# Kernel tuning notes

Hardware: AMD Instinct MI355X
Metric: run time of the kernel (lower is better)

Reference implementation:

```python
import jax, jax.numpy as jnp
import numpy as np


def setup_inputs() -> dict:
    key = jax.random.key(0)
    k1, k2, k3, k4, k5 = jax.random.split(key, 5)
    B, C, H, W = 8, 256, 64, 64
    Cp = C // 8  # query/key channels
    x = jax.random.normal(k1, (B, C, H, W), dtype=jnp.float32)
    # 1x1 conv weights (bias=False in the module), spectral norm treated as a fixed weight scale
    Wq = jax.random.normal(k2, (Cp, C), dtype=jnp.float32) * 0.05
    Wk = jax.random.normal(k3, (Cp, C), dtype=jnp.float32) * 0.05
    Wv = jax.random.normal(k4, (C, C), dtype=jnp.float32) * 0.05
    gamma = jax.random.normal(k5, (1,), dtype=jnp.float32)
    return {"x": x, "Wq": Wq, "Wk": Wk, "Wv": Wv, "gamma": gamma}


def reference(x, Wq, Wk, Wv, gamma):
    B, C, H, W = x.shape
    xf = x.reshape(B, C, H * W)  # (B, C, N)
    # ConvLayer = 1x1 conv (no bias) followed by ReLU
    f = jax.nn.relu(jnp.einsum('oc,bcn->bon', Wq, xf))  # (B, C', N)
    g = jax.nn.relu(jnp.einsum('oc,bcn->bon', Wk, xf))  # (B, C', N)
    h = jax.nn.relu(jnp.einsum('oc,bcn->bon', Wv, xf))  # (B, C, N)
    # beta = softmax(f^T g, dim=1): normalize over the FIRST N axis (faithful to source)
    scores = jnp.einsum('bcn,bcm->bnm', f, g)  # (B, N, N)
    beta = jax.nn.softmax(scores, axis=1)
    o = gamma * jnp.einsum('bcn,bnm->bcm', h, beta) + xf  # (B, C, N)
    return o.reshape(B, C, H, W)
```

## Files before the change

### kernel.cpp

```cpp
#include <hip/hip_runtime.h>


typedef __attribute__((ext_vector_type(8))) short bf16x8;
typedef __attribute__((ext_vector_type(4))) float f32x4;
typedef __attribute__((ext_vector_type(4))) unsigned short us4;

#define LOG2E 1.44269504088896f

static __device__ __forceinline__ unsigned short f2bf(float x) {
    union { float f; unsigned u; } v; v.f = x;
    unsigned r = v.u + 0x7FFFu + ((v.u >> 16) & 1u);
    return (unsigned short)(r >> 16);
}
static __device__ __forceinline__ float bf2f(unsigned short u) {
    union { unsigned u; float f; } v; v.u = ((unsigned)u) << 16;
    return v.f;
}

__global__ __launch_bounds__(256) void wconv_kernel(
    const float* __restrict__ Wq, const float* __restrict__ Wk,
    const float* __restrict__ Wv, unsigned short* __restrict__ wq,
    unsigned short* __restrict__ wk, unsigned short* __restrict__ wv)
{
    const int i = blockIdx.x * 256 + threadIdx.x;
    if (i < 8192)            wq[i] = f2bf(Wq[i] * LOG2E);
    else if (i < 16384)      wk[i - 8192] = f2bf(Wk[i - 8192]);
    else                     wv[i - 16384] = f2bf(Wv[i - 16384]);
}

#define XPITCH 264
#define HPITCH 72
__global__ __launch_bounds__(256, 2) void producer_kernel(
    const float* __restrict__ x, const unsigned short* __restrict__ wq,
    const unsigned short* __restrict__ wk, const unsigned short* __restrict__ wv,
    unsigned short* __restrict__ f_t, unsigned short* __restrict__ g_t,
    unsigned short* __restrict__ h_bf, float* __restrict__ normg,
    unsigned* __restrict__ maxnf_u)
{
    __shared__ unsigned short xh_s[256 * HPITCH];
    __shared__ unsigned short fg_s[4 * 2 * 512];

    const int tid  = threadIdx.x;
    const int w    = tid >> 6;
    const int lane = tid & 63;
    const int q    = lane >> 4;
    const int r    = lane & 15;
    const int b    = blockIdx.y;
    const int nt   = blockIdx.x;
    const int n0   = nt << 6;
    const size_t bN = (size_t)b << 12;
    const f32x4 zero = {0.f, 0.f, 0.f, 0.f};

#pragma unroll
    for (int jj = 0; jj < 4; jj++) {
        const int task = jj * 256 + tid;
        const int n4 = task & 15;
        const int c4 = task >> 4;
        float va[4][4];
#pragma unroll
        for (int i = 0; i < 4; i++) {
            const float4 v = ((const float4*)(x + ((size_t)b << 20)
                              + (size_t)(c4 * 4 + i) * 4096 + n0))[n4];
            va[i][0] = v.x; va[i][1] = v.y; va[i][2] = v.z; va[i][3] = v.w;
        }
#pragma unroll
        for (int i = 0; i < 4; i++) {
            us4 t;
            t.x = f2bf(va[0][i]); t.y = f2bf(va[1][i]);
            t.z = f2bf(va[2][i]); t.w = f2bf(va[3][i]);
            *(us4*)(xh_s + (n4 * 4 + i) * XPITCH + c4 * 4) = t;
        }
    }
    __syncthreads();

    f32x4 acch[4][4];
    f32x4 accf[2], accg[2];
#pragma unroll
    for (int cs = 0; cs < 4; cs++)
#pragma unroll
        for (int ns = 0; ns < 4; ns++) acch[cs][ns] = zero;
    accf[0] = accf[1] = accg[0] = accg[1] = zero;

    for (int ks = 0; ks < 8; ks++) {
        const int kof = ks * 32 + q * 8;
        bf16x8 av[4], aq[2], ak[2];
#pragma unroll
        for (int cs = 0; cs < 4; cs++)
            av[cs] = *(const bf16x8*)(wv + (size_t)(w * 64 + cs * 16 + r) * 256 + kof);
#pragma unroll
        for (int ms = 0; ms < 2; ms++) {
            aq[ms] = *(const bf16x8*)(wq + (size_t)(ms * 16 + r) * 256 + kof);
            ak[ms] = *(const bf16x8*)(wk + (size_t)(ms * 16 + r) * 256 + kof);
        }
#pragma unroll
        for (int ns = 0; ns < 4; ns++) {
            const bf16x8 bx = *(const bf16x8*)(xh_s + (ns * 16 + r) * XPITCH + kof);
#pragma unroll
            for (int cs = 0; cs < 4; cs++)
                acch[cs][ns] = __builtin_amdgcn_mfma_f32_16x16x32_bf16(av[cs], bx, acch[cs][ns], 0, 0, 0);
            if (ns == w) {
#pragma unroll
                for (int ms = 0; ms < 2; ms++) {
                    accf[ms] = __builtin_amdgcn_mfma_f32_16x16x32_bf16(aq[ms], bx, accf[ms], 0, 0, 0);
                    accg[ms] = __builtin_amdgcn_mfma_f32_16x16x32_bf16(ak[ms], bx, accg[ms], 0, 0, 0);
                }
            }
        }
    }

    unsigned short* lf = fg_s + w * 1024;
    unsigned short* lg = lf + 512;
#pragma unroll
    for (int ms = 0; ms < 2; ms++)
#pragma unroll
        for (int reg = 0; reg < 4; reg++) {
            lf[r * 32 + ms * 16 + q * 4 + reg] = f2bf(fmaxf(accf[ms][reg], 0.f));
            lg[r * 32 + ms * 16 + q * 4 + reg] = f2bf(fmaxf(accg[ms][reg], 0.f));
        }
    const bf16x8 ffrag = *(const bf16x8*)(lf + r * 32 + q * 8);
    const bf16x8 gfrag = *(const bf16x8*)(lg + r * 32 + q * 8);
    *(bf16x8*)(f_t + ((bN + n0 + w * 16 + r) << 5) + q * 8) = ffrag;
    *(bf16x8*)(g_t + ((bN + n0 + w * 16 + r) << 5) + q * 8) = gfrag;

    float nf2 = 0.f, ng2 = 0.f;
#pragma unroll
    for (int i = 0; i < 8; i++) {
        const float fv = bf2f(((unsigned short*)&ffrag)[i]);
        const float gv = bf2f(((unsigned short*)&gfrag)[i]);
        nf2 += fv * fv; ng2 += gv * gv;
    }
    nf2 += __shfl_xor(nf2, 16); nf2 += __shfl_xor(nf2, 32);
    ng2 += __shfl_xor(ng2, 16); ng2 += __shfl_xor(ng2, 32);
    if (q == 0) normg[bN + n0 + w * 16 + r] = sqrtf(ng2);
    float nf = sqrtf(nf2);
#pragma unroll
    for (int off = 1; off < 16; off <<= 1) nf = fmaxf(nf, __shfl_xor(nf, off));
    if (lane == 0) atomicMax(maxnf_u + b, __float_as_uint(nf));

    __syncthreads();
#pragma unroll
    for (int cs = 0; cs < 4; cs++)
#pragma unroll
        for (int ns = 0; ns < 4; ns++)
#pragma unroll
            for (int reg = 0; reg < 4; reg++)
                xh_s[(w * 64 + cs * 16 + q * 4 + reg) * HPITCH + ns * 16 + r] =
                    f2bf(fmaxf(acch[cs][ns][reg], 0.f));
    __syncthreads();
    const size_t hdst = ((size_t)(b * 64 + nt)) << 14;
#pragma unroll
    for (int p = 0; p < 8; p++) {
        const int c = p * 32 + (tid >> 3);
        const int k = tid & 7;
        *(bf16x8*)(h_bf + hdst + c * 64 + k * 8) =
            *(const bf16x8*)(xh_s + c * HPITCH + k * 8);
    }
}

__global__ __launch_bounds__(256, 2) void attn_kernel(
    const unsigned short* __restrict__ f_t, const unsigned short* __restrict__ g_t,
    const unsigned short* __restrict__ h_bf, const float* __restrict__ x,
    const float* __restrict__ gamma, const float* __restrict__ normg,
    const unsigned* __restrict__ maxnf_u, float* __restrict__ out)
{
    __shared__ unsigned short p_s[3][64 * 64];
    __shared__ float red_l[4][64];
    __shared__ float sLi[64];

    const int tid  = threadIdx.x;
    const int w    = tid >> 6;
    const int lane = tid & 63;
    const int q    = lane >> 4;
    const int r    = lane & 15;
    const int b    = blockIdx.y;
    const int m0   = blockIdx.x << 6;

    const size_t bN = (size_t)b << 12;
    const int c0 = w << 6;
    const f32x4 zero = {0.f, 0.f, 0.f, 0.f};

    bf16x8 bg[4];
    float nMh[4];
    const float mnf = __uint_as_float(maxnf_u[b]);
#pragma unroll
    for (int ms = 0; ms < 4; ms++) {
        bg[ms] = *(const bf16x8*)(g_t + ((bN + m0 + ms * 16 + r) << 5) + (q << 3));
        nMh[ms] = -(mnf * normg[bN + m0 + ms * 16 + r] * 1.0002f);
    }

    f32x4 acc[4][4];
#pragma unroll
    for (int cs = 0; cs < 4; cs++)
#pragma unroll
        for (int ms = 0; ms < 4; ms++) acc[cs][ms] = zero;
    float lt[4] = {0.f, 0.f, 0.f, 0.f};

    const int wkey = r & 7;
    const int wchunkoff = (((((w << 1) + (q >> 1)) ^ wkey) << 3)) + ((q & 1) << 2);
    const int rkoff0 = ((q ^ wkey) << 3);
    const int rkoff1 = (((4 + q) ^ wkey) << 3);

    auto ldf = [&](int t) {
        return *(const bf16x8*)(f_t + ((bN + (t << 6) + (w << 4) + r) << 5) + (q << 3));
    };
    auto produce = [&](const bf16x8 af, unsigned short* pb) {
#pragma unroll
        for (int ms = 0; ms < 4; ms++) {
            f32x4 ci; ci[0] = ci[1] = ci[2] = ci[3] = nMh[ms];
            const f32x4 sv = __builtin_amdgcn_mfma_f32_16x16x32_bf16(af, bg[ms], ci, 0, 0, 0);
            const float e0 = __builtin_amdgcn_exp2f(sv[0]);
            const float e1 = __builtin_amdgcn_exp2f(sv[1]);
            const float e2 = __builtin_amdgcn_exp2f(sv[2]);
            const float e3 = __builtin_amdgcn_exp2f(sv[3]);
            lt[ms] += (e0 + e1) + (e2 + e3);
            uint2 pk;
            pk.x = __builtin_amdgcn_perm(__float_as_uint(e1), __float_as_uint(e0), 0x07060302u);
            pk.y = __builtin_amdgcn_perm(__float_as_uint(e3), __float_as_uint(e2), 0x07060302u);
            *(uint2*)(pb + ((ms * 16 + r) << 6) + wchunkoff) = pk;
        }
    };

    bf16x8 afn = ldf(0);
    produce(afn, p_s[0]);
    afn = ldf(1);

    int sr = 0, sw = 1;
    for (int t = 0; t < 64; t++) {
        __syncthreads();
        const unsigned short* hb = h_bf + (((size_t)(b * 64 + t)) << 14);
        bf16x8 ah[8];
#pragma unroll
        for (int cs = 0; cs < 4; cs++) {
            const unsigned short* hp = hb + ((c0 + cs * 16 + r) << 6) + (q << 3);
            ah[cs * 2]     = *(const bf16x8*)(hp);
            ah[cs * 2 + 1] = *(const bf16x8*)(hp + 32);
        }
        if (t < 63) {
            const bf16x8 afc = afn;
            if (t < 62) afn = ldf(t + 2);
            produce(afc, p_s[sw]);
        }
        const unsigned short* pb = p_s[sr];
        bf16x8 bp[4][2];
#pragma unroll
        for (int ms = 0; ms < 4; ms++) {
            bp[ms][0] = *(const bf16x8*)(pb + ((ms * 16 + r) << 6) + rkoff0);
            bp[ms][1] = *(const bf16x8*)(pb + ((ms * 16 + r) << 6) + rkoff1);
        }
#pragma unroll
        for (int ch = 0; ch < 2; ch++)
#pragma unroll
            for (int cs = 0; cs < 4; cs++)
#pragma unroll
                for (int ms = 0; ms < 4; ms++)
                    acc[cs][ms] = __builtin_amdgcn_mfma_f32_16x16x32_bf16(
                        ah[cs * 2 + ch], bp[ms][ch], acc[cs][ms], 0, 0, 0);
        sr = sw;
        sw = (sw == 2) ? 0 : sw + 1;
    }

#pragma unroll
    for (int ms = 0; ms < 4; ms++) {
        lt[ms] += __shfl_xor(lt[ms], 16);
        lt[ms] += __shfl_xor(lt[ms], 32);
    }
    __syncthreads();
    if (q == 0)
#pragma unroll
        for (int ms = 0; ms < 4; ms++) red_l[w][ms * 16 + r] = lt[ms];
    __syncthreads();
    if (tid < 64)
        sLi[tid] = 1.f / (red_l[0][tid] + red_l[1][tid] + red_l[2][tid] + red_l[3][tid]);
    __syncthreads();

    const float gm = gamma[0];
#pragma unroll
    for (int cs = 0; cs < 4; cs++) {
#pragma unroll
        for (int ms = 0; ms < 4; ms++) {
            const float gl = gm * sLi[ms * 16 + r];
#pragma unroll
            for (int reg = 0; reg < 4; reg++) {
                const int c = c0 + cs * 16 + q * 4 + reg;
                const size_t a = (((size_t)b * 256 + c) << 12) + m0 + ms * 16 + r;
                out[a] = gl * acc[cs][ms][reg] + x[a];
            }
        }
    }
}

extern "C" void kernel_launch(void* const* d_in, const int* in_sizes, int n_in,
                              void* d_out, int out_size, void* d_ws, size_t ws_size,
                              hipStream_t stream) {
    const float* x     = (const float*)d_in[0];
    const float* Wq    = (const float*)d_in[1];
    const float* Wk    = (const float*)d_in[2];
    const float* Wv    = (const float*)d_in[3];
    const float* gamma = (const float*)d_in[4];
    float* out = (float*)d_out;

    char* ws = (char*)d_ws;
    unsigned short* f_t  = (unsigned short*)ws;
    unsigned short* g_t  = (unsigned short*)(ws + (2u << 20));
    unsigned short* h_bf = (unsigned short*)(ws + (4u << 20));
    float*          ng   = (float*)(ws + (20u << 20));
    unsigned*       mnf  = (unsigned*)(ws + (20u << 20) + (1u << 17));
    unsigned short* wq   = (unsigned short*)(ws + (21u << 20));
    unsigned short* wk   = wq + 8192;
    unsigned short* wv   = wk + 8192;

    hipMemsetAsync(mnf, 0, 8 * sizeof(unsigned), stream);
    wconv_kernel<<<dim3(320), 256, 0, stream>>>(Wq, Wk, Wv, wq, wk, wv);
    producer_kernel<<<dim3(64, 8), 256, 0, stream>>>(x, wq, wk, wv, f_t, g_t, h_bf, ng, mnf);
    attn_kernel<<<dim3(64, 8), 256, 0, stream>>>(f_t, g_t, h_bf, x, gamma, ng, mnf, out);
}
```

Baseline: 262.9 us.

## Replace atomic max with per-block partial maxima, interleave batches, nontemporal IO

The producer no longer uses atomicMax on a memset buffer. Each wave writes its partial max norm to a per-batch array, and the attention kernel reduces the 256 partials per batch with shuffles, so the memset launch goes away. Both kernels now use a 1D grid with batch in the low bits, which interleaves batches across CUs and changes L2 locality. The x loads and the output stores use nontemporal hints to avoid polluting the cache, at the cost of extra reduction work in every attention block.

```diff
diff --git a/kernel.cpp b/kernel.cpp
--- a/kernel.cpp
+++ b/kernel.cpp
@@ -35,7 +35,7 @@
     const unsigned short* __restrict__ wk, const unsigned short* __restrict__ wv,
     unsigned short* __restrict__ f_t, unsigned short* __restrict__ g_t,
     unsigned short* __restrict__ h_bf, float* __restrict__ normg,
-    unsigned* __restrict__ maxnf_u)
+    float* __restrict__ pmax)
 {
     __shared__ unsigned short xh_s[256 * HPITCH];
     __shared__ unsigned short fg_s[4 * 2 * 512];
@@ -45,8 +45,8 @@
     const int lane = tid & 63;
     const int q    = lane >> 4;
     const int r    = lane & 15;
-    const int b    = blockIdx.y;
-    const int nt   = blockIdx.x;
+    const int b    = blockIdx.x & 7;
+    const int nt   = blockIdx.x >> 3;
     const int n0   = nt << 6;
     const size_t bN = (size_t)b << 12;
     const f32x4 zero = {0.f, 0.f, 0.f, 0.f};
@@ -59,8 +59,9 @@
         float va[4][4];
 #pragma unroll
         for (int i = 0; i < 4; i++) {
-            const float4 v = ((const float4*)(x + ((size_t)b << 20)
-                              + (size_t)(c4 * 4 + i) * 4096 + n0))[n4];
+            const f32x4 v = __builtin_nontemporal_load(
+                (const f32x4*)(x + ((size_t)b << 20)
+                               + (size_t)(c4 * 4 + i) * 4096 + n0) + n4);
             va[i][0] = v.x; va[i][1] = v.y; va[i][2] = v.z; va[i][3] = v.w;
         }
 #pragma unroll
@@ -135,7 +136,7 @@
     float nf = sqrtf(nf2);
 #pragma unroll
     for (int off = 1; off < 16; off <<= 1) nf = fmaxf(nf, __shfl_xor(nf, off));
-    if (lane == 0) atomicMax(maxnf_u + b, __float_as_uint(nf));
+    if (lane == 0) pmax[(b << 8) + nt * 4 + w] = nf;
 
     __syncthreads();
 #pragma unroll
@@ -161,7 +162,7 @@
     const unsigned short* __restrict__ f_t, const unsigned short* __restrict__ g_t,
     const unsigned short* __restrict__ h_bf, const float* __restrict__ x,
     const float* __restrict__ gamma, const float* __restrict__ normg,
-    const unsigned* __restrict__ maxnf_u, float* __restrict__ out)
+    const float* __restrict__ pmax, float* __restrict__ out)
 {
     __shared__ unsigned short p_s[3][64 * 64];
     __shared__ float red_l[4][64];
@@ -172,16 +173,22 @@
     const int lane = tid & 63;
     const int q    = lane >> 4;
     const int r    = lane & 15;
-    const int b    = blockIdx.y;
-    const int m0   = blockIdx.x << 6;
+    const int b    = blockIdx.x & 7;
+    const int m0   = (blockIdx.x >> 3) << 6;
 
     const size_t bN = (size_t)b << 12;
     const int c0 = w << 6;
-    const f32x4 zero = {0.f, 0.f, 0.f, 0.f};
+
+    float pv = pmax[(b << 8) + lane];
+    pv = fmaxf(pv, pmax[(b << 8) + 64 + lane]);
+    pv = fmaxf(pv, pmax[(b << 8) + 128 + lane]);
+    pv = fmaxf(pv, pmax[(b << 8) + 192 + lane]);
+#pragma unroll
+    for (int off = 1; off < 64; off <<= 1) pv = fmaxf(pv, __shfl_xor(pv, off));
+    const float mnf = pv;
 
     bf16x8 bg[4];
     float nMh[4];
-    const float mnf = __uint_as_float(maxnf_u[b]);
 #pragma unroll
     for (int ms = 0; ms < 4; ms++) {
         bg[ms] = *(const bf16x8*)(g_t + ((bN + m0 + ms * 16 + r) << 5) + (q << 3));
@@ -189,6 +196,7 @@
     }
 
     f32x4 acc[4][4];
+    const f32x4 zero = {0.f, 0.f, 0.f, 0.f};
 #pragma unroll
     for (int cs = 0; cs < 4; cs++)
 #pragma unroll
@@ -283,7 +291,8 @@
             for (int reg = 0; reg < 4; reg++) {
                 const int c = c0 + cs * 16 + q * 4 + reg;
                 const size_t a = (((size_t)b * 256 + c) << 12) + m0 + ms * 16 + r;
-                out[a] = gl * acc[cs][ms][reg] + x[a];
+                const float xv = __builtin_nontemporal_load(x + a);
+                __builtin_nontemporal_store(gl * acc[cs][ms][reg] + xv, out + a);
             }
         }
     }
@@ -304,13 +313,12 @@
     unsigned short* g_t  = (unsigned short*)(ws + (2u << 20));
     unsigned short* h_bf = (unsigned short*)(ws + (4u << 20));
     float*          ng   = (float*)(ws + (20u << 20));
-    unsigned*       mnf  = (unsigned*)(ws + (20u << 20) + (1u << 17));
+    float*          pmx  = (float*)(ws + (20u << 20) + (1u << 17));
     unsigned short* wq   = (unsigned short*)(ws + (21u << 20));
     unsigned short* wk   = wq + 8192;
     unsigned short* wv   = wk + 8192;
 
-    hipMemsetAsync(mnf, 0, 8 * sizeof(unsigned), stream);
     wconv_kernel<<<dim3(320), 256, 0, stream>>>(Wq, Wk, Wv, wq, wk, wv);
-    producer_kernel<<<dim3(64, 8), 256, 0, stream>>>(x, wq, wk, wv, f_t, g_t, h_bf, ng, mnf);
-    attn_kernel<<<dim3(64, 8), 256, 0, stream>>>(f_t, g_t, h_bf, x, gamma, ng, mnf, out);
-}
+    producer_kernel<<<dim3(512), 256, 0, stream>>>(x, wq, wk, wv, f_t, g_t, h_bf, ng, pmx);
+    attn_kernel<<<dim3(512), 256, 0, stream>>>(f_t, g_t, h_bf, x, gamma, ng, pmx, out);
+}
```

New measurement: 250.6 us. 1.05x faster.
